# Kernel tuning notes

Hardware: AMD Instinct MI355X
Metric: run time of the kernel (lower is better)

## Reference

```python
import jax, jax.numpy as jnp
import numpy as np

B, S, V, F, H = 256, 512, 50000, 64, 256


def setup_inputs() -> dict:
    key = jax.random.key(0)
    ks = jax.random.split(key, 12)
    s_in = 1.0 / np.sqrt(F)
    s_hid = 1.0 / np.sqrt(H)
    return {
        "batch": jax.random.randint(ks[0], (B, S), 0, V),
        "features": jax.random.normal(ks[1], (V, F), jnp.float32),
        "W_ih0": jax.random.normal(ks[2], (H, F), jnp.float32) * s_in,
        "W_hh0": jax.random.normal(ks[3], (H, H), jnp.float32) * s_hid,
        "b_ih0": jax.random.normal(ks[4], (H,), jnp.float32) * s_hid,
        "b_hh0": jax.random.normal(ks[5], (H,), jnp.float32) * s_hid,
        "W_ih1": jax.random.normal(ks[6], (H, H), jnp.float32) * s_hid,
        "W_hh1": jax.random.normal(ks[7], (H, H), jnp.float32) * s_hid,
        "b_ih1": jax.random.normal(ks[8], (H,), jnp.float32) * s_hid,
        "b_hh1": jax.random.normal(ks[9], (H,), jnp.float32) * s_hid,
        "W_out": jax.random.normal(ks[10], (V, H), jnp.float32) * s_hid,
        "b_out": jax.random.normal(ks[11], (V,), jnp.float32) * s_hid,
    }


def _rnn_layer(x, W_ih, W_hh, b_ih, b_hh):
    # x: [B, S, Din] -> [B, S, H]; torch tanh RNN: h_t = tanh(x_t W_ih^T + b_ih + h_{t-1} W_hh^T + b_hh)
    xW = jnp.einsum('bsd,hd->bsh', x, W_ih) + (b_ih + b_hh)  # precompute input projection
    h0 = jnp.zeros((x.shape[0], W_hh.shape[0]), x.dtype)

    def step(h, xt):
        h = jnp.tanh(xt + h @ W_hh.T)
        return h, h

    _, ys = jax.lax.scan(step, h0, jnp.swapaxes(xW, 0, 1))  # scan over time
    return jnp.swapaxes(ys, 0, 1)


def reference(batch, features, W_ih0, W_hh0, b_ih0, b_hh0,
              W_ih1, W_hh1, b_ih1, b_hh1, W_out, b_out):
    # vectorized replacement of the nested per-token gather loop
    full_representation = features[batch]            # [B, S, F]
    h = _rnn_layer(full_representation, W_ih0, W_hh0, b_ih0, b_hh0)
    h = _rnn_layer(h, W_ih1, W_hh1, b_ih1, b_hh1)    # [B, S, H]
    return h[:, -1, :] @ W_out.T + b_out             # [B, V]
```

## Files before the change

### kernel.cpp

```cpp
#include <hip/hip_runtime.h>

#define B_ 256
#define S_ 512
#define V_ 50000
#define F_ 64
#define H_ 256

typedef _Float16 f16;
typedef _Float16 f16x2 __attribute__((ext_vector_type(2)));
typedef _Float16 f16x4 __attribute__((ext_vector_type(4)));
typedef _Float16 f16x8 __attribute__((ext_vector_type(8)));
typedef float f32x4 __attribute__((ext_vector_type(4)));

#define MFMA(a, b, c) __builtin_amdgcn_mfma_f32_16x16x32_f16((a), (b), (c), 0, 0, 0)

__device__ __forceinline__ f16x8 cvt8(const float4 a, const float4 b) {
    f16x8 v;
    v[0] = (f16)a.x; v[1] = (f16)a.y; v[2] = (f16)a.z; v[3] = (f16)a.w;
    v[4] = (f16)b.x; v[5] = (f16)b.y; v[6] = (f16)b.z; v[7] = (f16)b.w;
    return v;
}

__device__ __forceinline__ float fast_tanh(float x) {
    float e = __expf(2.f * x);
    float r = __builtin_amdgcn_rcpf(e + 1.f);
    return __builtin_fmaf(-2.f, r, 1.f);
}

__device__ __forceinline__ f32x4 cvt4f(const f16x4 v) {
    f32x4 r; r[0] = (float)v[0]; r[1] = (float)v[1]; r[2] = (float)v[2]; r[3] = (float)v[3];
    return r;
}
__device__ __forceinline__ f16x4 pack4(const f32x4 a, const f32x4 b) {
    f16x4 r; r[0] = (f16)(a[0] + b[0]); r[1] = (f16)(a[1] + b[1]);
    r[2] = (f16)(a[2] + b[2]); r[3] = (f16)(a[3] + b[3]);
    return r;
}
__device__ __forceinline__ f16x4 tanh4(const f32x4 a, const f32x4 b) {
    f16x4 r;
#pragma unroll
    for (int i = 0; i < 4; ++i) r[i] = (f16)fast_tanh(a[i] + b[i]);
    return r;
}

__global__ void k_init_flags(int* flags) {
    if (threadIdx.x < 128) flags[threadIdx.x] = 0;
}

__global__ __launch_bounds__(512) void k_vocab_proj(
    const float* __restrict__ feat, const float* __restrict__ Wih,
    const float* __restrict__ bi, const float* __restrict__ bh,
    f16* __restrict__ T)
{
    __shared__ char Wl[256 * 128];
    __shared__ char Xl[16 * 128];
    const int tid = threadIdx.x;
    {
        const int n = tid >> 1, k0 = (tid & 1) << 5;
#pragma unroll
        for (int k = k0; k < k0 + 32; k += 8) {
            float4 a = *(const float4*)(Wih + n * F_ + k);
            float4 b = *(const float4*)(Wih + n * F_ + k + 4);
            *(f16x8*)(Wl + n * 128 + (((k >> 3) ^ (n & 7)) << 4)) = cvt8(a, b);
        }
    }
    const int v0 = blockIdx.x * 16;
    {
        const int m = tid >> 5, k = (tid & 31) << 1;
        float2 a = *(const float2*)(feat + (v0 + m) * F_ + k);
        f16x2 v; v[0] = (f16)a.x; v[1] = (f16)a.y;
        *(f16x2*)(Xl + m * 128 + ((((k >> 3) ^ (m & 7)) << 4) | ((k & 7) << 1))) = v;
    }
    __syncthreads();
    const int lane = tid & 63, w = tid >> 6;
    const int q = lane & 15, g = lane >> 4;
#pragma unroll
    for (int nt = 0; nt < 2; ++nt) {
        const int n0 = w * 32 + nt * 16;
        const int nrow = n0 + q;
        float4 b1 = *(const float4*)(bi + n0 + g * 4);
        float4 b2 = *(const float4*)(bh + n0 + g * 4);
        f32x4 acc = {b1.x + b2.x, b1.y + b2.y, b1.z + b2.z, b1.w + b2.w};
#pragma unroll
        for (int kb = 0; kb < 2; ++kb) {
            f16x8 a = *(const f16x8*)(Wl + nrow * 128 + (((kb * 4 + g) ^ (nrow & 7)) << 4));
            f16x8 b = *(const f16x8*)(Xl + q * 128 + (((kb * 4 + g) ^ (q & 7)) << 4));
            acc = MFMA(a, b, acc);
        }
        f16x4 o; o[0] = (f16)acc[0]; o[1] = (f16)acc[1]; o[2] = (f16)acc[2]; o[3] = (f16)acc[3];
        *(f16x4*)(T + (size_t)(v0 + q) * H_ + n0 + g * 4) = o;
    }
}

__global__ __launch_bounds__(512) __attribute__((amdgpu_waves_per_eu(2, 2)))
void k_rnn_split(
    const f16* __restrict__ T, const int* __restrict__ idx,
    const float* __restrict__ Whh0, const float* __restrict__ Wih1,
    const float* __restrict__ bih1, const float* __restrict__ bhh1,
    const float* __restrict__ Whh1,
    f16* __restrict__ pbuf, int* flags, f16* __restrict__ h1out)
{
    __shared__ char hb[2][8192];
    const int wg = blockIdx.x;
    const int tid = threadIdx.x, lane = tid & 63, w = tid >> 6;
    const int q = lane & 15, g = lane >> 4;
    const int ncol = w * 32;
    const int swz = (q & 7) << 4;

    int rbase[2], wbase[2];
#pragma unroll
    for (int p2 = 0; p2 < 2; ++p2)
        rbase[p2] = q * 512 + ((p2 * 64 + g * 16) ^ swz);
#pragma unroll
    for (int tt = 0; tt < 2; ++tt)
        wbase[tt] = q * 512 + (((ncol + tt * 16 + g * 4) * 2) ^ swz);

    const int pr = (wg < 16) ? wg : wg - 16;
    const int brow = pr * 16 + q;
    const size_t prow = (size_t)brow * 512;

#define FRD(kb_, RD_) (*(const f16x8*)(hb[RD_] + rbase[(kb_) & 1] + (((kb_) >> 1) * 128)))
#define HWR(tt_, WR_) (*(f16x4*)(hb[WR_] + wbase[tt_]))
#define STEP_BAR() do { \
        asm volatile("s_waitcnt lgkmcnt(0)" ::: "memory"); \
        __builtin_amdgcn_s_barrier(); \
    } while (0)

    if (wg < 16) {
        f16x8 wA[2][8], wP[2][8];
#pragma unroll
        for (int tt = 0; tt < 2; ++tt) {
            const int n = ncol + tt * 16 + q;
#pragma unroll
            for (int kb = 0; kb < 8; ++kb) {
                const int o = n * H_ + kb * 32 + g * 8;
                wA[tt][kb] = cvt8(*(const float4*)(Whh0 + o), *(const float4*)(Whh0 + o + 4));
                wP[tt][kb] = cvt8(*(const float4*)(Wih1 + o), *(const float4*)(Wih1 + o + 4));
            }
        }
        f32x4 bs1[2];
#pragma unroll
        for (int tt = 0; tt < 2; ++tt) {
            const int n = ncol + tt * 16 + g * 4;
            float4 x = *(const float4*)(bih1 + n);
            float4 y = *(const float4*)(bhh1 + n);
            bs1[tt][0] = x.x + y.x; bs1[tt][1] = x.y + y.y;
            bs1[tt][2] = x.z + y.z; bs1[tt][3] = x.w + y.w;
        }
        {
            f32x4 z = {0.f, 0.f, 0.f, 0.f};
            *(f32x4*)(hb[1] + tid * 16) = z;
        }
        const int* idxr = idx + brow * S_;
        int* myflag = flags + wg * 8 + w;
        f16x4 xa[2], xb[2];
        {
            const size_t r0 = (size_t)idxr[0] * H_, r1 = (size_t)idxr[1] * H_;
#pragma unroll
            for (int tt = 0; tt < 2; ++tt) {
                xa[tt] = *(const f16x4*)(T + r0 + ncol + tt * 16 + g * 4);
                xb[tt] = *(const f16x4*)(T + r1 + ncol + tt * 16 + g * 4);
            }
        }
        int iA = idxr[2], iB = idxr[3];
        __syncthreads();

#define PBODY(XV, ID, RD, WR, T_) do {                                          \
                \
        f16x8 bf0 = FRD(0, RD), bf1 = FRD(1, RD), bf2 = FRD(2, RD),             \
              bf3 = FRD(3, RD), bf4 = FRD(4, RD), bf5 = FRD(5, RD),             \
              bf6 = FRD(6, RD), bf7 = FRD(7, RD);                               \
        f32x4 aL[2], aH[2];                                                     \
        _Pragma("unroll")                                                       \
        for (int tt = 0; tt < 2; ++tt) {                                        \
            aL[tt] = cvt4f(XV[tt]);                                             \
            aH[tt][0] = 0.f; aH[tt][1] = 0.f; aH[tt][2] = 0.f; aH[tt][3] = 0.f; \
        }                                                                       \
        {                 \
            const size_t rr = (size_t)ID * H_;                                  \
            _Pragma("unroll")                                                   \
            for (int tt = 0; tt < 2; ++tt)                                      \
                XV[tt] = *(const f16x4*)(T + rr + ncol + tt * 16 + g * 4);      \
            const int t4 = ((T_) + 4 < S_) ? (T_) + 4 : S_ - 1;                 \
            ID = idxr[t4];                                                      \
        }                                                                       \
                                               \
        _Pragma("unroll")                                                       \
        for (int tt = 0; tt < 2; ++tt) {                                        \
            aL[tt] = MFMA(wA[tt][0], bf0, aL[tt]);                              \
            aH[tt] = MFMA(wA[tt][4], bf4, aH[tt]);                              \
            aL[tt] = MFMA(wA[tt][1], bf1, aL[tt]);                              \
            aH[tt] = MFMA(wA[tt][5], bf5, aH[tt]);                              \
            aL[tt] = MFMA(wA[tt][2], bf2, aL[tt]);                              \
            aH[tt] = MFMA(wA[tt][6], bf6, aH[tt]);                              \
            aL[tt] = MFMA(wA[tt][3], bf3, aL[tt]);                              \
            aH[tt] = MFMA(wA[tt][7], bf7, aH[tt]);                              \
        }                                                                       \
                                  \
        _Pragma("unroll")                                                       \
        for (int tt = 0; tt < 2; ++tt) HWR(tt, WR) = tanh4(aL[tt], aH[tt]);     \
                  \
        f32x4 pL[2], pH[2];                                                     \
        _Pragma("unroll")                                                       \
        for (int tt = 0; tt < 2; ++tt) {                                        \
            pL[tt] = bs1[tt];                                                   \
            pH[tt][0] = 0.f; pH[tt][1] = 0.f; pH[tt][2] = 0.f; pH[tt][3] = 0.f; \
            pL[tt] = MFMA(wP[tt][0], bf0, pL[tt]);                              \
            pH[tt] = MFMA(wP[tt][4], bf4, pH[tt]);                              \
            pL[tt] = MFMA(wP[tt][1], bf1, pL[tt]);                              \
            pH[tt] = MFMA(wP[tt][5], bf5, pH[tt]);                              \
            pL[tt] = MFMA(wP[tt][2], bf2, pL[tt]);                              \
            pH[tt] = MFMA(wP[tt][6], bf6, pH[tt]);                              \
            pL[tt] = MFMA(wP[tt][3], bf3, pL[tt]);                              \
            pH[tt] = MFMA(wP[tt][7], bf7, pH[tt]);                              \
            *(f16x4*)(pbuf + (prow + (T_) - 1) * 256 + ncol + tt * 16 + g * 4)  \
                = pack4(pL[tt], pH[tt]);                                        \
        }                                                                       \
        if ((((T_) & 7) == 0) && lane == 0)                                     \
            __hip_atomic_store(myflag, (T_), __ATOMIC_RELEASE,                  \
                               __HIP_MEMORY_SCOPE_AGENT);                       \
        STEP_BAR();                                                             \
    } while (0)

        {
            f16x8 bf0 = FRD(0, 1), bf1 = FRD(1, 1), bf2 = FRD(2, 1), bf3 = FRD(3, 1),
                  bf4 = FRD(4, 1), bf5 = FRD(5, 1), bf6 = FRD(6, 1), bf7 = FRD(7, 1);
            f32x4 aL[2], aH[2];
#pragma unroll
            for (int tt = 0; tt < 2; ++tt) {
                aL[tt] = cvt4f(xa[tt]);
                aH[tt][0] = 0.f; aH[tt][1] = 0.f; aH[tt][2] = 0.f; aH[tt][3] = 0.f;
            }
            {
                const size_t rr = (size_t)iA * H_;
#pragma unroll
                for (int tt = 0; tt < 2; ++tt)
                    xa[tt] = *(const f16x4*)(T + rr + ncol + tt * 16 + g * 4);
                iA = idxr[4];
            }
#pragma unroll
            for (int tt = 0; tt < 2; ++tt) {
                aL[tt] = MFMA(wA[tt][0], bf0, aL[tt]);
                aH[tt] = MFMA(wA[tt][4], bf4, aH[tt]);
                aL[tt] = MFMA(wA[tt][1], bf1, aL[tt]);
                aH[tt] = MFMA(wA[tt][5], bf5, aH[tt]);
                aL[tt] = MFMA(wA[tt][2], bf2, aL[tt]);
                aH[tt] = MFMA(wA[tt][6], bf6, aH[tt]);
                aL[tt] = MFMA(wA[tt][3], bf3, aL[tt]);
                aH[tt] = MFMA(wA[tt][7], bf7, aH[tt]);
                HWR(tt, 0) = tanh4(aL[tt], aH[tt]);
            }
            STEP_BAR();
        }
        for (int t = 1; t < 511; t += 2) {
            PBODY(xb, iB, 0, 1, t);
            PBODY(xa, iA, 1, 0, t + 1);
        }
        PBODY(xb, iB, 0, 1, 511);
        {
            f16x8 bf0 = FRD(0, 1), bf1 = FRD(1, 1), bf2 = FRD(2, 1), bf3 = FRD(3, 1),
                  bf4 = FRD(4, 1), bf5 = FRD(5, 1), bf6 = FRD(6, 1), bf7 = FRD(7, 1);
            f32x4 pL[2], pH[2];
#pragma unroll
            for (int tt = 0; tt < 2; ++tt) {
                pL[tt] = bs1[tt];
                pH[tt][0] = 0.f; pH[tt][1] = 0.f; pH[tt][2] = 0.f; pH[tt][3] = 0.f;
                pL[tt] = MFMA(wP[tt][0], bf0, pL[tt]);
                pH[tt] = MFMA(wP[tt][4], bf4, pH[tt]);
                pL[tt] = MFMA(wP[tt][1], bf1, pL[tt]);
                pH[tt] = MFMA(wP[tt][5], bf5, pH[tt]);
                pL[tt] = MFMA(wP[tt][2], bf2, pL[tt]);
                pH[tt] = MFMA(wP[tt][6], bf6, pH[tt]);
                pL[tt] = MFMA(wP[tt][3], bf3, pL[tt]);
                pH[tt] = MFMA(wP[tt][7], bf7, pH[tt]);
                *(f16x4*)(pbuf + (prow + 511) * 256 + ncol + tt * 16 + g * 4)
                    = pack4(pL[tt], pH[tt]);
            }
        }
        if (lane == 0)
            __hip_atomic_store(myflag, 512, __ATOMIC_RELEASE, __HIP_MEMORY_SCOPE_AGENT);
#undef PBODY
    } else {
        f16x8 wC[2][8];
#pragma unroll
        for (int tt = 0; tt < 2; ++tt) {
            const int n = ncol + tt * 16 + q;
#pragma unroll
            for (int kb = 0; kb < 8; ++kb) {
                const int o = n * H_ + kb * 32 + g * 8;
                wC[tt][kb] = cvt8(*(const float4*)(Whh1 + o), *(const float4*)(Whh1 + o + 4));
            }
        }
        {   f32x4 z = {0.f, 0.f, 0.f, 0.f}; *(f32x4*)(hb[1] + tid * 16) = z; }
        const int* fl = flags + pr * 8;
        __syncthreads();

#define SPIN(need) do {                                                         \
        int mn;                                                                 \
        do {                                                                    \
            mn = 0x7fffffff;                                                    \
            _Pragma("unroll")                                                   \
            for (int i = 0; i < 8; ++i) {                                       \
                int v = __hip_atomic_load(fl + i, __ATOMIC_RELAXED,             \
                                          __HIP_MEMORY_SCOPE_AGENT);            \
                mn = v < mn ? v : mn;                                           \
            }                                                                   \
        } while (mn < (need));                                                  \
        __builtin_amdgcn_fence(__ATOMIC_ACQUIRE, "agent");                      \
    } while (0)

#define CBODY(PV, RD, WR, T_) do {                                              \
        f16x8 cf0 = FRD(0, RD), cf1 = FRD(1, RD), cf2 = FRD(2, RD),             \
              cf3 = FRD(3, RD), cf4 = FRD(4, RD), cf5 = FRD(5, RD),             \
              cf6 = FRD(6, RD), cf7 = FRD(7, RD);                               \
        f32x4 aL[2], aH[2];                                                     \
        _Pragma("unroll")                                                       \
        for (int tt = 0; tt < 2; ++tt) {                                        \
            aL[tt] = cvt4f(PV[tt]);                                             \
            aH[tt][0] = 0.f; aH[tt][1] = 0.f; aH[tt][2] = 0.f; aH[tt][3] = 0.f; \
        }                                                                       \
        {                                                                       \
            const int tr = ((T_) + 2 < S_) ? (T_) + 2 : S_ - 1;                 \
            _Pragma("unroll")                                                   \
            for (int tt = 0; tt < 2; ++tt)                                      \
                PV[tt] = *(const f16x4*)(pbuf + (prow + tr) * 256 + ncol + tt * 16 + g * 4); \
        }                                                                       \
        _Pragma("unroll")                                                       \
        for (int tt = 0; tt < 2; ++tt) {                                        \
            aL[tt] = MFMA(wC[tt][0], cf0, aL[tt]);                              \
            aH[tt] = MFMA(wC[tt][4], cf4, aH[tt]);                              \
            aL[tt] = MFMA(wC[tt][1], cf1, aL[tt]);                              \
            aH[tt] = MFMA(wC[tt][5], cf5, aH[tt]);                              \
            aL[tt] = MFMA(wC[tt][2], cf2, aL[tt]);                              \
            aH[tt] = MFMA(wC[tt][6], cf6, aH[tt]);                              \
            aL[tt] = MFMA(wC[tt][3], cf3, aL[tt]);                              \
            aH[tt] = MFMA(wC[tt][7], cf7, aH[tt]);                              \
        }                                                                       \
        _Pragma("unroll")                                                       \
        for (int tt = 0; tt < 2; ++tt) {                                        \
            f16x4 hv = tanh4(aL[tt], aH[tt]);                                   \
            HWR(tt, WR) = hv;                                                   \
            if ((T_) == S_ - 1)                                                 \
                *(f16x4*)(h1out + (size_t)brow * H_ + ncol + tt * 16 + g * 4) = hv; \
        }                                                                       \
        STEP_BAR();                                                             \
    } while (0)

        f16x4 pa[2], pb[2];
        SPIN(6);
#pragma unroll
        for (int tt = 0; tt < 2; ++tt) {
            pa[tt] = *(const f16x4*)(pbuf + (prow + 0) * 256 + ncol + tt * 16 + g * 4);
            pb[tt] = *(const f16x4*)(pbuf + (prow + 1) * 256 + ncol + tt * 16 + g * 4);
        }
        for (int tb = 0; tb < 512; tb += 4) {
            if (tb) {
                const int need = (tb + 6 < 512) ? tb + 6 : 512;
                SPIN(need);
            }
            CBODY(pa, 1, 0, tb);
            CBODY(pb, 0, 1, tb + 1);
            CBODY(pa, 1, 0, tb + 2);
            CBODY(pb, 0, 1, tb + 3);
        }
#undef CBODY
#undef SPIN
    }
#undef FRD
#undef HWR
#undef STEP_BAR
}

__global__ __launch_bounds__(512) void k_out(
    const f16* __restrict__ h1, const float* __restrict__ Wout,
    const float* __restrict__ bout, float* __restrict__ out)
{
    __shared__ char Hl[256 * 512];
    const int tid = threadIdx.x;
    {
        const int m = tid >> 1, half = tid & 1;
#pragma unroll
        for (int i = 0; i < 16; ++i) {
            const int blk = half * 16 + i;
            f16x8 v = *(const f16x8*)(h1 + m * H_ + blk * 8);
            *(f16x8*)(Hl + m * 512 + ((blk ^ (m & 7)) << 4)) = v;
        }
    }
    __syncthreads();
    const int lane = tid & 63, w = tid >> 6;
    const int q = lane & 15, g = lane >> 4;
    const int v0 = blockIdx.x * 80;
    f32x4 acc[5][2];
#pragma unroll
    for (int vt = 0; vt < 5; ++vt) {
        float4 bo = *(const float4*)(bout + v0 + vt * 16 + g * 4);
#pragma unroll
        for (int bt = 0; bt < 2; ++bt) {
            acc[vt][bt][0] = bo.x; acc[vt][bt][1] = bo.y;
            acc[vt][bt][2] = bo.z; acc[vt][bt][3] = bo.w;
        }
    }
#pragma unroll
    for (int kb = 0; kb < 8; ++kb) {
        f16x8 bf[2];
#pragma unroll
        for (int bt = 0; bt < 2; ++bt) {
            const int mrow = (w * 2 + bt) * 16 + q;
            bf[bt] = *(const f16x8*)(Hl + mrow * 512 + (((kb * 4 + g) ^ (mrow & 7)) << 4));
        }
#pragma unroll
        for (int vt = 0; vt < 5; ++vt) {
            const size_t vrow = v0 + vt * 16 + q;
            float4 a = *(const float4*)(Wout + vrow * H_ + kb * 32 + g * 8);
            float4 b = *(const float4*)(Wout + vrow * H_ + kb * 32 + g * 8 + 4);
            f16x8 af = cvt8(a, b);
#pragma unroll
            for (int bt = 0; bt < 2; ++bt)
                acc[vt][bt] = MFMA(af, bf[bt], acc[vt][bt]);
        }
    }
#pragma unroll
    for (int vt = 0; vt < 5; ++vt)
#pragma unroll
        for (int bt = 0; bt < 2; ++bt) {
            const int b = (w * 2 + bt) * 16 + q;
            const int v = v0 + vt * 16 + g * 4;
            float4 o = {acc[vt][bt][0], acc[vt][bt][1], acc[vt][bt][2], acc[vt][bt][3]};
            *(float4*)(out + (size_t)b * V_ + v) = o;
        }
}

extern "C" void kernel_launch(void* const* d_in, const int* in_sizes, int n_in,
                              void* d_out, int out_size, void* d_ws, size_t ws_size,
                              hipStream_t stream) {
    (void)in_sizes; (void)n_in; (void)out_size; (void)ws_size;
    const int*   batch = (const int*)  d_in[0];
    const float* feat  = (const float*)d_in[1];
    const float* Wih0  = (const float*)d_in[2];
    const float* Whh0  = (const float*)d_in[3];
    const float* bih0  = (const float*)d_in[4];
    const float* bhh0  = (const float*)d_in[5];
    const float* Wih1  = (const float*)d_in[6];
    const float* Whh1  = (const float*)d_in[7];
    const float* bih1  = (const float*)d_in[8];
    const float* bhh1  = (const float*)d_in[9];
    const float* Wout  = (const float*)d_in[10];
    const float* bout  = (const float*)d_in[11];
    float* out = (float*)d_out;

    f16* T     = (f16*)d_out;
    int* flags = (int*)((char*)d_out + 48000000);
    f16* pbuf  = (f16*)d_ws;
    f16* h1out = (f16*)((char*)d_ws + (size_t)B_ * S_ * H_ * 2);

    k_init_flags<<<dim3(1), dim3(128), 0, stream>>>(flags);
    k_vocab_proj<<<dim3(V_ / 16), dim3(512), 0, stream>>>(feat, Wih0, bih0, bhh0, T);
    k_rnn_split<<<dim3(32), dim3(512), 0, stream>>>(T, batch, Whh0, Wih1, bih1, bhh1,
                                                    Whh1, pbuf, flags, h1out);
    k_out<<<dim3(625), dim3(512), 0, stream>>>(h1out, Wout, bout, out);
}
```

Baseline: 934.5 us.

## Split layer-1 input projection into separate projector workgroups via h0 ring buffer

Restructures the recurrent kernel into three roles. Layer-0 workgroups now only run the recurrence and write h0 into a 128-step ring buffer. 128 new projector workgroups compute the Wih1 input projection from that ring, and layer-1 workgroups consume the projected values. This takes the extra 16 MFMAs per step off the serial layer-0 critical path and spreads them across more CUs. In exchange it adds global ring traffic, more flag polling, back-pressure spins, and coarser consumer sync granularity.

New measurement: 1.125 ms. +20.3%, slower.

```diff
diff --git a/kernel.cpp b/kernel.cpp
--- a/kernel.cpp
+++ b/kernel.cpp
@@ -44,7 +44,7 @@
 }
 
 __global__ void k_init_flags(int* flags) {
-    if (threadIdx.x < 128) flags[threadIdx.x] = 0;
+    if (threadIdx.x < 256) flags[threadIdx.x] = 0;
 }
 
 __global__ __launch_bounds__(512) void k_vocab_proj(
@@ -93,31 +93,31 @@
 }
 
 __global__ __launch_bounds__(512) __attribute__((amdgpu_waves_per_eu(2, 2)))
-void k_rnn_split(
+void k_rnn3(
     const f16* __restrict__ T, const int* __restrict__ idx,
     const float* __restrict__ Whh0, const float* __restrict__ Wih1,
     const float* __restrict__ bih1, const float* __restrict__ bhh1,
     const float* __restrict__ Whh1,
-    f16* __restrict__ pbuf, int* flags, f16* __restrict__ h1out)
+    f16* __restrict__ h0ring, f16* __restrict__ pbufp,
+    int* flags, f16* __restrict__ h1out)
 {
     __shared__ char hb[2][8192];
     const int wg = blockIdx.x;
     const int tid = threadIdx.x, lane = tid & 63, w = tid >> 6;
-    const int q = lane & 15, g = lane >> 4;
+    const int q = lane & 15, gl = lane >> 4;
     const int ncol = w * 32;
     const int swz = (q & 7) << 4;
 
     int rbase[2], wbase[2];
 #pragma unroll
     for (int p2 = 0; p2 < 2; ++p2)
-        rbase[p2] = q * 512 + ((p2 * 64 + g * 16) ^ swz);
+        rbase[p2] = q * 512 + ((p2 * 64 + gl * 16) ^ swz);
 #pragma unroll
     for (int tt = 0; tt < 2; ++tt)
-        wbase[tt] = q * 512 + (((ncol + tt * 16 + g * 4) * 2) ^ swz);
-
-    const int pr = (wg < 16) ? wg : wg - 16;
-    const int brow = pr * 16 + q;
-    const size_t prow = (size_t)brow * 512;
+        wbase[tt] = q * 512 + (((ncol + tt * 16 + gl * 4) * 2) ^ swz);
+
+    int* prodf = flags;
+    int* projf = flags + 128;
 
 #define FRD(kb_, RD_) (*(const f16x8*)(hb[RD_] + rbase[(kb_) & 1] + (((kb_) >> 1) * 128)))
 #define HWR(tt_, WR_) (*(f16x4*)(hb[WR_] + wbase[tt_]))
@@ -125,48 +125,50 @@
         asm volatile("s_waitcnt lgkmcnt(0)" ::: "memory"); \
         __builtin_amdgcn_s_barrier(); \
     } while (0)
+#define PCOV(gr_, cv_) do {                                                     \
+        int f_[8];                                                              \
+        _Pragma("unroll")                                                       \
+        for (int i_ = 0; i_ < 8; ++i_)                                          \
+            f_[i_] = __hip_atomic_load(projf + (gr_) * 8 + i_, __ATOMIC_RELAXED,\
+                                       __HIP_MEMORY_SCOPE_AGENT);               \
+        cv_ = f_[0];                                                            \
+        _Pragma("unroll")                                                       \
+        for (int i_ = 1; i_ < 8; ++i_) cv_ = (cv_ == i_ * 64) ? f_[i_] : cv_;   \
+    } while (0)
 
     if (wg < 16) {
-        f16x8 wA[2][8], wP[2][8];
+        const int gr = wg;
+        const int brow = gr * 16 + q;
+        f16x8 wA[2][8];
 #pragma unroll
         for (int tt = 0; tt < 2; ++tt) {
             const int n = ncol + tt * 16 + q;
 #pragma unroll
             for (int kb = 0; kb < 8; ++kb) {
-                const int o = n * H_ + kb * 32 + g * 8;
+                const int o = n * H_ + kb * 32 + gl * 8;
                 wA[tt][kb] = cvt8(*(const float4*)(Whh0 + o), *(const float4*)(Whh0 + o + 4));
-                wP[tt][kb] = cvt8(*(const float4*)(Wih1 + o), *(const float4*)(Wih1 + o + 4));
-            }
-        }
-        f32x4 bs1[2];
-#pragma unroll
-        for (int tt = 0; tt < 2; ++tt) {
-            const int n = ncol + tt * 16 + g * 4;
-            float4 x = *(const float4*)(bih1 + n);
-            float4 y = *(const float4*)(bhh1 + n);
-            bs1[tt][0] = x.x + y.x; bs1[tt][1] = x.y + y.y;
-            bs1[tt][2] = x.z + y.z; bs1[tt][3] = x.w + y.w;
-        }
-        {
-            f32x4 z = {0.f, 0.f, 0.f, 0.f};
-            *(f32x4*)(hb[1] + tid * 16) = z;
-        }
+            }
+        }
+        {   f32x4 z = {0.f, 0.f, 0.f, 0.f}; *(f32x4*)(hb[1] + tid * 16) = z; }
         const int* idxr = idx + brow * S_;
-        int* myflag = flags + wg * 8 + w;
+        int* myflag = prodf + gr * 8 + w;
         f16x4 xa[2], xb[2];
         {
             const size_t r0 = (size_t)idxr[0] * H_, r1 = (size_t)idxr[1] * H_;
 #pragma unroll
             for (int tt = 0; tt < 2; ++tt) {
-                xa[tt] = *(const f16x4*)(T + r0 + ncol + tt * 16 + g * 4);
-                xb[tt] = *(const f16x4*)(T + r1 + ncol + tt * 16 + g * 4);
+                xa[tt] = *(const f16x4*)(T + r0 + ncol + tt * 16 + gl * 4);
+                xb[tt] = *(const f16x4*)(T + r1 + ncol + tt * 16 + gl * 4);
             }
         }
         int iA = idxr[2], iB = idxr[3];
         __syncthreads();
 
 #define PBODY(XV, ID, RD, WR, T_) do {                                          \
-                \
+        if (((T_) & 15) == 0) {    \
+            int cv_;                                                            \
+            do { PCOV(gr, cv_); } while (cv_ < (T_) - 97);                      \
+        }                                                                       \
         f16x8 bf0 = FRD(0, RD), bf1 = FRD(1, RD), bf2 = FRD(2, RD),             \
               bf3 = FRD(3, RD), bf4 = FRD(4, RD), bf5 = FRD(5, RD),             \
               bf6 = FRD(6, RD), bf7 = FRD(7, RD);                               \
@@ -176,15 +178,14 @@
             aL[tt] = cvt4f(XV[tt]);                                             \
             aH[tt][0] = 0.f; aH[tt][1] = 0.f; aH[tt][2] = 0.f; aH[tt][3] = 0.f; \
         }                                                                       \
-        {                 \
+        {                                                                       \
             const size_t rr = (size_t)ID * H_;                                  \
             _Pragma("unroll")                                                   \
             for (int tt = 0; tt < 2; ++tt)                                      \
-                XV[tt] = *(const f16x4*)(T + rr + ncol + tt * 16 + g * 4);      \
+                XV[tt] = *(const f16x4*)(T + rr + ncol + tt * 16 + gl * 4);     \
             const int t4 = ((T_) + 4 < S_) ? (T_) + 4 : S_ - 1;                 \
             ID = idxr[t4];                                                      \
         }                                                                       \
-                                               \
         _Pragma("unroll")                                                       \
         for (int tt = 0; tt < 2; ++tt) {                                        \
             aL[tt] = MFMA(wA[tt][0], bf0, aL[tt]);                              \
@@ -196,25 +197,12 @@
             aL[tt] = MFMA(wA[tt][3], bf3, aL[tt]);                              \
             aH[tt] = MFMA(wA[tt][7], bf7, aH[tt]);                              \
         }                                                                       \
-                                  \
-        _Pragma("unroll")                                                       \
-        for (int tt = 0; tt < 2; ++tt) HWR(tt, WR) = tanh4(aL[tt], aH[tt]);     \
-                  \
-        f32x4 pL[2], pH[2];                                                     \
+        const size_t rs = ((size_t)(gr * 128 + ((T_) & 127)) * 16 + q) * 256;   \
         _Pragma("unroll")                                                       \
         for (int tt = 0; tt < 2; ++tt) {                                        \
-            pL[tt] = bs1[tt];                                                   \
-            pH[tt][0] = 0.f; pH[tt][1] = 0.f; pH[tt][2] = 0.f; pH[tt][3] = 0.f; \
-            pL[tt] = MFMA(wP[tt][0], bf0, pL[tt]);                              \
-            pH[tt] = MFMA(wP[tt][4], bf4, pH[tt]);                              \
-            pL[tt] = MFMA(wP[tt][1], bf1, pL[tt]);                              \
-            pH[tt] = MFMA(wP[tt][5], bf5, pH[tt]);                              \
-            pL[tt] = MFMA(wP[tt][2], bf2, pL[tt]);                              \
-            pH[tt] = MFMA(wP[tt][6], bf6, pH[tt]);                              \
-            pL[tt] = MFMA(wP[tt][3], bf3, pL[tt]);                              \
-            pH[tt] = MFMA(wP[tt][7], bf7, pH[tt]);                              \
-            *(f16x4*)(pbuf + (prow + (T_) - 1) * 256 + ncol + tt * 16 + g * 4)  \
-                = pack4(pL[tt], pH[tt]);                                        \
+            f16x4 hv = tanh4(aL[tt], aH[tt]);                                   \
+            HWR(tt, WR) = hv;                                                   \
+            *(f16x4*)(h0ring + rs + ncol + tt * 16 + gl * 4) = hv;              \
         }                                                                       \
         if ((((T_) & 7) == 0) && lane == 0)                                     \
             __hip_atomic_store(myflag, (T_), __ATOMIC_RELEASE,                  \
@@ -235,7 +223,7 @@
                 const size_t rr = (size_t)iA * H_;
 #pragma unroll
                 for (int tt = 0; tt < 2; ++tt)
-                    xa[tt] = *(const f16x4*)(T + rr + ncol + tt * 16 + g * 4);
+                    xa[tt] = *(const f16x4*)(T + rr + ncol + tt * 16 + gl * 4);
                 iA = idxr[4];
             }
 #pragma unroll
@@ -248,7 +236,13 @@
                 aH[tt] = MFMA(wA[tt][6], bf6, aH[tt]);
                 aL[tt] = MFMA(wA[tt][3], bf3, aL[tt]);
                 aH[tt] = MFMA(wA[tt][7], bf7, aH[tt]);
-                HWR(tt, 0) = tanh4(aL[tt], aH[tt]);
+            }
+            const size_t rs = ((size_t)(gr * 128) * 16 + q) * 256;
+#pragma unroll
+            for (int tt = 0; tt < 2; ++tt) {
+                f16x4 hv = tanh4(aL[tt], aH[tt]);
+                HWR(tt, 0) = hv;
+                *(f16x4*)(h0ring + rs + ncol + tt * 16 + gl * 4) = hv;
             }
             STEP_BAR();
         }
@@ -257,55 +251,29 @@
             PBODY(xa, iA, 1, 0, t + 1);
         }
         PBODY(xb, iB, 0, 1, 511);
-        {
-            f16x8 bf0 = FRD(0, 1), bf1 = FRD(1, 1), bf2 = FRD(2, 1), bf3 = FRD(3, 1),
-                  bf4 = FRD(4, 1), bf5 = FRD(5, 1), bf6 = FRD(6, 1), bf7 = FRD(7, 1);
-            f32x4 pL[2], pH[2];
-#pragma unroll
-            for (int tt = 0; tt < 2; ++tt) {
-                pL[tt] = bs1[tt];
-                pH[tt][0] = 0.f; pH[tt][1] = 0.f; pH[tt][2] = 0.f; pH[tt][3] = 0.f;
-                pL[tt] = MFMA(wP[tt][0], bf0, pL[tt]);
-                pH[tt] = MFMA(wP[tt][4], bf4, pH[tt]);
-                pL[tt] = MFMA(wP[tt][1], bf1, pL[tt]);
-                pH[tt] = MFMA(wP[tt][5], bf5, pH[tt]);
-                pL[tt] = MFMA(wP[tt][2], bf2, pL[tt]);
-                pH[tt] = MFMA(wP[tt][6], bf6, pH[tt]);
-                pL[tt] = MFMA(wP[tt][3], bf3, pL[tt]);
-                pH[tt] = MFMA(wP[tt][7], bf7, pH[tt]);
-                *(f16x4*)(pbuf + (prow + 511) * 256 + ncol + tt * 16 + g * 4)
-                    = pack4(pL[tt], pH[tt]);
-            }
-        }
         if (lane == 0)
             __hip_atomic_store(myflag, 512, __ATOMIC_RELEASE, __HIP_MEMORY_SCOPE_AGENT);
 #undef PBODY
-    } else {
+    } else if (wg < 32) {
+        const int gr = wg - 16;
+        const int brow = gr * 16 + q;
+        const size_t prow = (size_t)brow * 512;
         f16x8 wC[2][8];
 #pragma unroll
         for (int tt = 0; tt < 2; ++tt) {
             const int n = ncol + tt * 16 + q;
 #pragma unroll
             for (int kb = 0; kb < 8; ++kb) {
-                const int o = n * H_ + kb * 32 + g * 8;
+                const int o = n * H_ + kb * 32 + gl * 8;
                 wC[tt][kb] = cvt8(*(const float4*)(Whh1 + o), *(const float4*)(Whh1 + o + 4));
             }
         }
         {   f32x4 z = {0.f, 0.f, 0.f, 0.f}; *(f32x4*)(hb[1] + tid * 16) = z; }
-        const int* fl = flags + pr * 8;
         __syncthreads();
 
 #define SPIN(need) do {                                                         \
-        int mn;                                                                 \
-        do {                                                                    \
-            mn = 0x7fffffff;                                                    \
-            _Pragma("unroll")                                                   \
-            for (int i = 0; i < 8; ++i) {                                       \
-                int v = __hip_atomic_load(fl + i, __ATOMIC_RELAXED,             \
-                                          __HIP_MEMORY_SCOPE_AGENT);            \
-                mn = v < mn ? v : mn;                                           \
-            }                                                                   \
-        } while (mn < (need));                                                  \
+        int cv_;                                                                \
+        do { PCOV(gr, cv_); } while (cv_ < (need));                             \
         __builtin_amdgcn_fence(__ATOMIC_ACQUIRE, "agent");                      \
     } while (0)
 
@@ -323,7 +291,7 @@
             const int tr = ((T_) + 2 < S_) ? (T_) + 2 : S_ - 1;                 \
             _Pragma("unroll")                                                   \
             for (int tt = 0; tt < 2; ++tt)                                      \
-                PV[tt] = *(const f16x4*)(pbuf + (prow + tr) * 256 + ncol + tt * 16 + g * 4); \
+                PV[tt] = *(const f16x4*)(pbufp + (prow + tr) * 256 + ncol + tt * 16 + gl * 4); \
         }                                                                       \
         _Pragma("unroll")                                                       \
         for (int tt = 0; tt < 2; ++tt) {                                        \
@@ -341,21 +309,21 @@
             f16x4 hv = tanh4(aL[tt], aH[tt]);                                   \
             HWR(tt, WR) = hv;                                                   \
             if ((T_) == S_ - 1)                                                 \
-                *(f16x4*)(h1out + (size_t)brow * H_ + ncol + tt * 16 + g * 4) = hv; \
+                *(f16x4*)(h1out + (size_t)brow * H_ + ncol + tt * 16 + gl * 4) = hv; \
         }                                                                       \
         STEP_BAR();                                                             \
     } while (0)
 
         f16x4 pa[2], pb[2];
-        SPIN(6);
+        SPIN(18);
 #pragma unroll
         for (int tt = 0; tt < 2; ++tt) {
-            pa[tt] = *(const f16x4*)(pbuf + (prow + 0) * 256 + ncol + tt * 16 + g * 4);
-            pb[tt] = *(const f16x4*)(pbuf + (prow + 1) * 256 + ncol + tt * 16 + g * 4);
+            pa[tt] = *(const f16x4*)(pbufp + (prow + 0) * 256 + ncol + tt * 16 + gl * 4);
+            pb[tt] = *(const f16x4*)(pbufp + (prow + 1) * 256 + ncol + tt * 16 + gl * 4);
         }
         for (int tb = 0; tb < 512; tb += 4) {
-            if (tb) {
-                const int need = (tb + 6 < 512) ? tb + 6 : 512;
+            if (tb && ((tb & 15) == 0)) {
+                const int need = (tb + 18 < 512) ? tb + 18 : 512;
                 SPIN(need);
             }
             CBODY(pa, 1, 0, tb);
@@ -365,7 +333,82 @@
         }
 #undef CBODY
 #undef SPIN
-    }
+    } else {
+        const int j = wg - 32;
+        const int gr = j >> 3, ed = j & 7;
+        f16x8 wP[2][8];
+#pragma unroll
+        for (int tt = 0; tt < 2; ++tt) {
+            const int n = ncol + tt * 16 + q;
+#pragma unroll
+            for (int kb = 0; kb < 8; ++kb) {
+                const int o = n * H_ + kb * 32 + gl * 8;
+                wP[tt][kb] = cvt8(*(const float4*)(Wih1 + o), *(const float4*)(Wih1 + o + 4));
+            }
+        }
+        f32x4 bs1[2];
+#pragma unroll
+        for (int tt = 0; tt < 2; ++tt) {
+            const int n = ncol + tt * 16 + gl * 4;
+            float4 x = *(const float4*)(bih1 + n);
+            float4 y = *(const float4*)(bhh1 + n);
+            bs1[tt][0] = x.x + y.x; bs1[tt][1] = x.y + y.y;
+            bs1[tt][2] = x.z + y.z; bs1[tt][3] = x.w + y.w;
+        }
+        const size_t crow = (size_t)(gr * 16 + q) * 512;
+        for (int tc = 0; tc < 4; ++tc) {
+            const int tb = ed * 64 + tc * 16;
+            {
+                int mn;
+                do {
+                    mn = 0x7fffffff;
+#pragma unroll
+                    for (int i = 0; i < 8; ++i) {
+                        int v = __hip_atomic_load(prodf + gr * 8 + i, __ATOMIC_RELAXED,
+                                                  __HIP_MEMORY_SCOPE_AGENT);
+                        mn = v < mn ? v : mn;
+                    }
+                } while (mn < tb + 15);
+            }
+            __builtin_amdgcn_fence(__ATOMIC_ACQUIRE, "agent");
+#pragma unroll 2
+            for (int mt = 0; mt < 16; ++mt) {
+                const int t = tb + mt;
+                const size_t rb = ((size_t)(gr * 128 + (t & 127)) * 16 + q) * 256 + gl * 8;
+                f16x8 b0 = *(const f16x8*)(h0ring + rb + 0 * 32);
+                f16x8 b1 = *(const f16x8*)(h0ring + rb + 1 * 32);
+                f16x8 b2 = *(const f16x8*)(h0ring + rb + 2 * 32);
+                f16x8 b3 = *(const f16x8*)(h0ring + rb + 3 * 32);
+                f16x8 b4 = *(const f16x8*)(h0ring + rb + 4 * 32);
+                f16x8 b5 = *(const f16x8*)(h0ring + rb + 5 * 32);
+                f16x8 b6 = *(const f16x8*)(h0ring + rb + 6 * 32);
+                f16x8 b7 = *(const f16x8*)(h0ring + rb + 7 * 32);
+                f32x4 pL[2], pH[2];
+#pragma unroll
+                for (int tt = 0; tt < 2; ++tt) {
+                    pL[tt] = bs1[tt];
+                    pH[tt][0] = 0.f; pH[tt][1] = 0.f; pH[tt][2] = 0.f; pH[tt][3] = 0.f;
+                    pL[tt] = MFMA(wP[tt][0], b0, pL[tt]);
+                    pH[tt] = MFMA(wP[tt][4], b4, pH[tt]);
+                    pL[tt] = MFMA(wP[tt][1], b1, pL[tt]);
+                    pH[tt] = MFMA(wP[tt][5], b5, pH[tt]);
+                    pL[tt] = MFMA(wP[tt][2], b2, pL[tt]);
+                    pH[tt] = MFMA(wP[tt][6], b6, pH[tt]);
+                    pL[tt] = MFMA(wP[tt][3], b3, pL[tt]);
+                    pH[tt] = MFMA(wP[tt][7], b7, pH[tt]);
+                }
+                const size_t ob = (crow + t) * 256;
+#pragma unroll
+                for (int tt = 0; tt < 2; ++tt)
+                    *(f16x4*)(pbufp + ob + ncol + tt * 16 + gl * 4) = pack4(pL[tt], pH[tt]);
+            }
+            __syncthreads();
+            if (tid == 0)
+                __hip_atomic_store(projf + gr * 8 + ed, tb + 16, __ATOMIC_RELEASE,
+                                   __HIP_MEMORY_SCOPE_AGENT);
+        }
+    }
+#undef PCOV
 #undef FRD
 #undef HWR
 #undef STEP_BAR
@@ -448,14 +491,15 @@
     const float* bout  = (const float*)d_in[11];
     float* out = (float*)d_out;
 
-    f16* T     = (f16*)d_out;
-    int* flags = (int*)((char*)d_out + 48000000);
-    f16* pbuf  = (f16*)d_ws;
-    f16* h1out = (f16*)((char*)d_ws + (size_t)B_ * S_ * H_ * 2);
-
-    k_init_flags<<<dim3(1), dim3(128), 0, stream>>>(flags);
+    f16* T      = (f16*)d_out;
+    f16* h0ring = (f16*)((char*)d_out + 27000000);
+    int* flags  = (int*)((char*)d_out + 48000000);
+    f16* pbufp  = (f16*)d_ws;
+    f16* h1out  = (f16*)((char*)d_ws + (size_t)B_ * S_ * H_ * 2);
+
+    k_init_flags<<<dim3(1), dim3(256), 0, stream>>>(flags);
     k_vocab_proj<<<dim3(V_ / 16), dim3(512), 0, stream>>>(feat, Wih0, bih0, bhh0, T);
-    k_rnn_split<<<dim3(32), dim3(512), 0, stream>>>(T, batch, Whh0, Wih1, bih1, bhh1,
-                                                    Whh1, pbuf, flags, h1out);
+    k_rnn3<<<dim3(160), dim3(512), 0, stream>>>(T, batch, Whh0, Wih1, bih1, bhh1,
+                                                Whh1, h0ring, pbufp, flags, h1out);
     k_out<<<dim3(625), dim3(512), 0, stream>>>(h1out, Wout, bout, out);
 }
```
